# Optimization experiments

Hardware: AMD Instinct MI355X
Metric: run time of the kernel (lower is better)

Reference implementation:

```python
import jax, jax.numpy as jnp
import numpy as np

FIX_SIGMA = (1.0, 2.0, 4.0, 8.0, 16.0)


def setup_inputs() -> dict:
    key = jax.random.key(0)
    k1, k2 = jax.random.split(key)
    B, C, D = 512, 32, 512
    source = jax.random.normal(k1, (B, C, D), dtype=jnp.float32)
    target = jax.random.normal(k2, (B, C, D), dtype=jnp.float32)
    return {"source": source, "target": target}


def _mmd(source, target):
    B = source.shape[0]
    total = jnp.concatenate([source, target], axis=0)  # [N, C, D], N = 2B
    # Pairwise per-channel squared L2 distance via norm expansion
    # (mathematically identical to ((x_i - x_j)**2).sum(-1), no [N,N,C,D] intermediate)
    sq = jnp.sum(total * total, axis=-1)  # [N, C]
    cross = jnp.einsum("icd,jcd->ijc", total, total)  # [N, N, C]
    L2 = sq[:, None, :] + sq[None, :, :] - 2.0 * cross  # [N, N, C]
    kernels = sum(jnp.exp(-L2 / sigma) for sigma in FIX_SIGMA)  # [N, N, C]
    XX = kernels[:B, :B, :]
    YY = kernels[B:, B:, :]
    XY = kernels[:B, B:, :]
    YX = kernels[B:, :B, :]
    loss_1 = XX + YY - XY - YX  # [B, B, C]
    # mean over dim0, mean over dim0 again (i.e. both batch dims), sum over channels
    return jnp.sum(jnp.mean(loss_1, axis=(0, 1)))


def reference(source, target):
    return _mmd(source, target)
```

## Files before the change

kernel.cpp:

```cpp
#include <hip/hip_runtime.h>

namespace {

constexpr int kC = 32;
constexpr int kD = 512;
constexpr int kB = 512;
constexpr int kN = 1024;
constexpr int kCD = kC * kD;
constexpr int BM = 128;
constexpr int BK = 32;
constexpr int KSTEPS = kD / BK;
constexpr int TILES = kN / BM;
constexpr int NPAIRS = TILES * (TILES + 1) / 2;

typedef float f32x4 __attribute__((ext_vector_type(4)));
typedef short s16x8 __attribute__((ext_vector_type(8)));

__device__ inline unsigned int pack_bf16(float a, float b) {
  unsigned int ua = __float_as_uint(a);
  unsigned int ub = __float_as_uint(b);
  ua += 0x7fffu + ((ua >> 16) & 1u);
  ub += 0x7fffu + ((ub >> 16) & 1u);
  return (ua >> 16) | (ub & 0xffff0000u);
}

__global__ void prep_kernel(const float* __restrict__ src,
                            const float* __restrict__ tgt,
                            float* __restrict__ sq,
                            unsigned int* __restrict__ tot,
                            float* __restrict__ out) {
  if (blockIdx.x == 0 && threadIdx.x == 0) *out = 0.f;
  int gw = (blockIdx.x * blockDim.x + threadIdx.x) >> 6;
  int lane = threadIdx.x & 63;
  int i = gw >> 5;
  int c = gw & 31;
  const float* p = (i < kB ? src + (size_t)i * kCD
                           : tgt + (size_t)(i - kB) * kCD) + c * kD;
  f32x4 v0 = *(const f32x4*)(p + lane * 8);
  f32x4 v1 = *(const f32x4*)(p + lane * 8 + 4);

  uint4 w = make_uint4(pack_bf16(v0.x, v0.y), pack_bf16(v0.z, v0.w),
                       pack_bf16(v1.x, v1.y), pack_bf16(v1.z, v1.w));
  *(uint4*)(tot + (size_t)(c * kN + i) * (kD / 2) + lane * 4) = w;

  float s = v0.x * v0.x + v0.y * v0.y + v0.z * v0.z + v0.w * v0.w
          + v1.x * v1.x + v1.y * v1.y + v1.z * v1.z + v1.w * v1.w;
#pragma unroll
  for (int o = 32; o > 0; o >>= 1) s += __shfl_down(s, o);
  if (lane == 0) sq[c * kN + i] = s;
}

__launch_bounds__(256, 4)
__global__ void mmd_kernel(const unsigned short* __restrict__ tot,
                           const float* __restrict__ sq,
                           float* __restrict__ out) {
  int b = blockIdx.x;
  int c = b & 31;
  int p = b >> 5;
  int ti = 0;
  while (p >= TILES - ti) { p -= TILES - ti; ++ti; }
  int tj = ti + p;

  __shared__ __align__(16) unsigned short lA[2][BM * BK];
  __shared__ __align__(16) unsigned short lB[2][BM * BK];
  __shared__ float wsum[4];

  const int t = threadIdx.x;
  const int lane = t & 63;
  const int wid = t >> 6;
  const int wr = wid >> 1;
  const int wc = wid & 1;

  const unsigned short* gA = tot + (size_t)(c * kN + ti * BM) * kD;
  const unsigned short* gB = tot + (size_t)(c * kN + tj * BM) * kD;

  const int srow = ((lane >> 3) << 1) + ((lane >> 2) & 1);
  const int scch = (lane & 3) ^ ((lane >> 3) & 3);

  auto STAGE = [&](int buf, int ks) {
#pragma unroll
    for (int q = 0; q < 2; ++q) {
      int i = wid * 2 + q;
      int r = 16 * i + srow;
      const unsigned short* sa = gA + (size_t)r * kD + ks * BK + scch * 8;
      const unsigned short* sb = gB + (size_t)r * kD + ks * BK + scch * 8;
      __builtin_amdgcn_global_load_lds(
          (const __attribute__((address_space(1))) unsigned int*)sa,
          (__attribute__((address_space(3))) unsigned int*)&lA[buf][i * 512],
          16, 0, 0);
      __builtin_amdgcn_global_load_lds(
          (const __attribute__((address_space(1))) unsigned int*)sb,
          (__attribute__((address_space(3))) unsigned int*)&lB[buf][i * 512],
          16, 0, 0);
    }
  };

  const int l15 = lane & 15;
  const int s4 = lane >> 4;
  const int laneoff = ((l15 >> 1) << 7) + ((l15 & 1) << 6) +
                      ((s4 ^ ((l15 >> 1) & 3)) << 4);

  f32x4 acc[4][4] = {};

  STAGE(0, 0);
  __syncthreads();

  int cur = 0;
  for (int ks = 0; ks < KSTEPS; ++ks) {
    if (ks + 1 < KSTEPS) STAGE(cur ^ 1, ks + 1);

    const char* Abase = (const char*)lA[cur] + wr * 4096 + laneoff;
    const char* Bbase = (const char*)lB[cur] + wc * 4096 + laneoff;
    s16x8 aF[4], bF[4];
#pragma unroll
    for (int m = 0; m < 4; ++m) aF[m] = *(const s16x8*)(Abase + m * 1024);
#pragma unroll
    for (int n = 0; n < 4; ++n) bF[n] = *(const s16x8*)(Bbase + n * 1024);
#pragma unroll
    for (int m = 0; m < 4; ++m)
#pragma unroll
      for (int n = 0; n < 4; ++n)
        acc[m][n] = __builtin_amdgcn_mfma_f32_16x16x32_bf16(
            aF[m], bF[n], acc[m][n], 0, 0, 0);

    __syncthreads();
    cur ^= 1;
  }

  const float sA = (ti < TILES / 2) ? 1.f : -1.f;
  const float sB = (tj < TILES / 2) ? 1.f : -1.f;
  const float scale = sA * sB * ((ti == tj) ? 1.f : 2.f) / 262144.f;
  const float* sqA = sq + c * kN + ti * BM;
  const float* sqB = sq + c * kN + tj * BM;

  float local = 0.f;
#pragma unroll
  for (int m = 0; m < 4; ++m) {
    float sqa_r[4];
#pragma unroll
    for (int rI = 0; rI < 4; ++rI)
      sqa_r[rI] = sqA[wr * 64 + m * 16 + (lane >> 4) * 4 + rI];
#pragma unroll
    for (int n = 0; n < 4; ++n) {
      float sqb_ = sqB[wc * 64 + n * 16 + (lane & 15)];
#pragma unroll
      for (int rI = 0; rI < 4; ++rI) {
        float L2 = sqa_r[rI] + sqb_ - 2.f * acc[m][n][rI];
        float tt = __expf(L2 * -0.0625f);
        float t2 = tt * tt, t4 = t2 * t2, t8 = t4 * t4;
        local += tt + t2 + t4 + t8 + t8 * t8;
      }
    }
  }

#pragma unroll
  for (int o = 32; o > 0; o >>= 1) local += __shfl_down(local, o);
  if (lane == 0) wsum[wid] = local;
  __syncthreads();
  if (t == 0)
    atomicAdd(out, (wsum[0] + wsum[1] + wsum[2] + wsum[3]) * scale);
}

}

extern "C" void kernel_launch(void* const* d_in, const int* in_sizes, int n_in,
                              void* d_out, int out_size, void* d_ws,
                              size_t ws_size, hipStream_t stream) {
  const float* src = (const float*)d_in[0];
  const float* tgt = (const float*)d_in[1];
  float* out = (float*)d_out;

  float* sq = (float*)d_ws;
  unsigned int* tot = (unsigned int*)((char*)d_ws + (size_t)kC * kN * 4);

  {
    int blocks = (kN * kC) / 4;
    prep_kernel<<<blocks, 256, 0, stream>>>(src, tgt, sq, tot, out);
  }
  {
    mmd_kernel<<<NPAIRS * kC, 256, 0, stream>>>((const unsigned short*)tot, sq, out);
  }
}
```

Baseline: 53.80 us.

## Give each wave its own 64x64 tile pair and load fragments directly from global

Replaces the 128x128 block tile with per-wave 64x64 tile pairs, so each of the four waves computes an independent triangle tile and scales its own partial sum. The LDS double-buffered staging and the per-step barriers are removed; MFMA fragments are loaded directly from global memory with a fully unrolled K loop. This is meant to cut synchronization and LDS traffic and to shrink upper-triangle waste with finer tiles, at the cost of more global/L2 traffic (less reuse per loaded row) and higher register pressure (launch bounds lowered to 3 blocks).

```diff
diff --git a/kernel.cpp b/kernel.cpp
--- a/kernel.cpp
+++ b/kernel.cpp
@@ -7,11 +7,10 @@
 constexpr int kB = 512;
 constexpr int kN = 1024;
 constexpr int kCD = kC * kD;
-constexpr int BM = 128;
-constexpr int BK = 32;
-constexpr int KSTEPS = kD / BK;
-constexpr int TILES = kN / BM;
-constexpr int NPAIRS = TILES * (TILES + 1) / 2;
+constexpr int TW = 64;
+constexpr int T2 = kN / TW;
+constexpr int NP = T2 * (T2 + 1) / 2;
+constexpr int KSTEPS = kD / 32;
 
 typedef float f32x4 __attribute__((ext_vector_type(4)));
 typedef short s16x8 __attribute__((ext_vector_type(8)));
@@ -50,88 +49,57 @@
   if (lane == 0) sq[c * kN + i] = s;
 }
 
-__launch_bounds__(256, 4)
+__launch_bounds__(256, 3)
 __global__ void mmd_kernel(const unsigned short* __restrict__ tot,
                            const float* __restrict__ sq,
                            float* __restrict__ out) {
-  int b = blockIdx.x;
-  int c = b & 31;
-  int p = b >> 5;
-  int ti = 0;
-  while (p >= TILES - ti) { p -= TILES - ti; ++ti; }
-  int tj = ti + p;
-
-  __shared__ __align__(16) unsigned short lA[2][BM * BK];
-  __shared__ __align__(16) unsigned short lB[2][BM * BK];
-  __shared__ float wsum[4];
-
+  const int b = blockIdx.x;
+  const int c = b & 31;
+  const int pg = b >> 5;
   const int t = threadIdx.x;
   const int lane = t & 63;
   const int wid = t >> 6;
-  const int wr = wid >> 1;
-  const int wc = wid & 1;
 
-  const unsigned short* gA = tot + (size_t)(c * kN + ti * BM) * kD;
-  const unsigned short* gB = tot + (size_t)(c * kN + tj * BM) * kD;
+  int p = pg * 4 + wid;
+  int ti = 0;
+  while (p >= T2 - ti) { p -= T2 - ti; ++ti; }
+  int tj = ti + p;
 
-  const int srow = ((lane >> 3) << 1) + ((lane >> 2) & 1);
-  const int scch = (lane & 3) ^ ((lane >> 3) & 3);
+  const unsigned short* gA = tot + (size_t)(c * kN + ti * TW) * kD;
+  const unsigned short* gB = tot + (size_t)(c * kN + tj * TW) * kD;
 
-  auto STAGE = [&](int buf, int ks) {
+  const int loff = (lane & 15) * kD + (lane >> 4) * 8;
+
+  const s16x8* aB[4];
+  const s16x8* bB[4];
 #pragma unroll
-    for (int q = 0; q < 2; ++q) {
-      int i = wid * 2 + q;
-      int r = 16 * i + srow;
-      const unsigned short* sa = gA + (size_t)r * kD + ks * BK + scch * 8;
-      const unsigned short* sb = gB + (size_t)r * kD + ks * BK + scch * 8;
-      __builtin_amdgcn_global_load_lds(
-          (const __attribute__((address_space(1))) unsigned int*)sa,
-          (__attribute__((address_space(3))) unsigned int*)&lA[buf][i * 512],
-          16, 0, 0);
-      __builtin_amdgcn_global_load_lds(
-          (const __attribute__((address_space(1))) unsigned int*)sb,
-          (__attribute__((address_space(3))) unsigned int*)&lB[buf][i * 512],
-          16, 0, 0);
-    }
-  };
-
-  const int l15 = lane & 15;
-  const int s4 = lane >> 4;
-  const int laneoff = ((l15 >> 1) << 7) + ((l15 & 1) << 6) +
-                      ((s4 ^ ((l15 >> 1) & 3)) << 4);
+  for (int m = 0; m < 4; ++m) {
+    aB[m] = (const s16x8*)(gA + (size_t)m * 16 * kD + loff);
+    bB[m] = (const s16x8*)(gB + (size_t)m * 16 * kD + loff);
+  }
 
   f32x4 acc[4][4] = {};
 
-  STAGE(0, 0);
-  __syncthreads();
-
-  int cur = 0;
+#pragma unroll
   for (int ks = 0; ks < KSTEPS; ++ks) {
-    if (ks + 1 < KSTEPS) STAGE(cur ^ 1, ks + 1);
-
-    const char* Abase = (const char*)lA[cur] + wr * 4096 + laneoff;
-    const char* Bbase = (const char*)lB[cur] + wc * 4096 + laneoff;
     s16x8 aF[4], bF[4];
 #pragma unroll
-    for (int m = 0; m < 4; ++m) aF[m] = *(const s16x8*)(Abase + m * 1024);
+    for (int m = 0; m < 4; ++m) aF[m] = aB[m][ks * 4];
 #pragma unroll
-    for (int n = 0; n < 4; ++n) bF[n] = *(const s16x8*)(Bbase + n * 1024);
+    for (int n = 0; n < 4; ++n) bF[n] = bB[n][ks * 4];
 #pragma unroll
     for (int m = 0; m < 4; ++m)
 #pragma unroll
       for (int n = 0; n < 4; ++n)
         acc[m][n] = __builtin_amdgcn_mfma_f32_16x16x32_bf16(
             aF[m], bF[n], acc[m][n], 0, 0, 0);
-
-    __syncthreads();
-    cur ^= 1;
   }
 
-  const float sA = (ti < TILES / 2) ? 1.f : -1.f;
-  const float sB = (tj < TILES / 2) ? 1.f : -1.f;
+  const float sA = (ti < T2 / 2) ? 1.f : -1.f;
+  const float sB = (tj < T2 / 2) ? 1.f : -1.f;
   const float scale = sA * sB * ((ti == tj) ? 1.f : 2.f) / 262144.f;
-  const float* sqA = sq + c * kN + ti * BM;
-  const float* sqB = sq + c * kN + tj * BM;
+  const float* sqA = sq + c * kN + ti * TW;
+  const float* sqB = sq + c * kN + tj * TW;
 
   float local = 0.f;
 #pragma unroll
@@ -139,10 +107,10 @@
     float sqa_r[4];
 #pragma unroll
     for (int rI = 0; rI < 4; ++rI)
-      sqa_r[rI] = sqA[wr * 64 + m * 16 + (lane >> 4) * 4 + rI];
+      sqa_r[rI] = sqA[m * 16 + (lane >> 4) * 4 + rI];
 #pragma unroll
     for (int n = 0; n < 4; ++n) {
-      float sqb_ = sqB[wc * 64 + n * 16 + (lane & 15)];
+      float sqb_ = sqB[n * 16 + (lane & 15)];
 #pragma unroll
       for (int rI = 0; rI < 4; ++rI) {
         float L2 = sqa_r[rI] + sqb_ - 2.f * acc[m][n][rI];
@@ -152,13 +120,15 @@
       }
     }
   }
+  local *= scale;
 
+  __shared__ float wsum[4];
 #pragma unroll
   for (int o = 32; o > 0; o >>= 1) local += __shfl_down(local, o);
   if (lane == 0) wsum[wid] = local;
   __syncthreads();
   if (t == 0)
-    atomicAdd(out, (wsum[0] + wsum[1] + wsum[2] + wsum[3]) * scale);
+    atomicAdd(out, wsum[0] + wsum[1] + wsum[2] + wsum[3]);
 }
 
 }
@@ -178,6 +148,7 @@
     prep_kernel<<<blocks, 256, 0, stream>>>(src, tgt, sq, tot, out);
   }
   {
-    mmd_kernel<<<NPAIRS * kC, 256, 0, stream>>>((const unsigned short*)tot, sq, out);
+    int blocks = NP * kC / 4;
+    mmd_kernel<<<blocks, 256, 0, stream>>>((const unsigned short*)tot, sq, out);
   }
 }
```

After: 95.88 us. 1.78x slower.
